# Optimization experiments

Measured on AMD Instinct MI355X. Metric: run time of the kernel, lower is better.

Reference implementation:

```python
import jax, jax.numpy as jnp
import numpy as np

B, N, S = 32, 4096, 11          # batch, n_inputs (64x64 feature map), n_slots
D_IN, D, MLP = 512, 512, 2048   # input feat dim, qkv_size, mlp hidden
ITERS = 3                       # num_iterations
EPS_ATTN = 1e-8                 # renormalize epsilon
EPS_LN = 1e-5                   # torch LayerNorm default eps


def layer_norm(x, g, b, eps=EPS_LN):
    mu = jnp.mean(x, axis=-1, keepdims=True)
    var = jnp.mean(jnp.square(x - mu), axis=-1, keepdims=True)
    return (x - mu) * jax.lax.rsqrt(var + eps) * g + b


def setup_inputs() -> dict:
    key = jax.random.key(0)
    ks = jax.random.split(key, 16)
    s = 0.02
    return {
        "slots": jax.random.normal(ks[0], (B, S, D), jnp.float32),
        "inputs": jax.random.normal(ks[1], (B, N, D_IN), jnp.float32),
        # input LayerNorm
        "ln_in_g": jnp.ones((D_IN,), jnp.float32),
        "ln_in_b": jnp.zeros((D_IN,), jnp.float32),
        # k / v projections (with bias, like nn.Linear)
        "Wk": jax.random.normal(ks[2], (D_IN, D), jnp.float32) * s,
        "bk": jnp.zeros((D,), jnp.float32),
        "Wv": jax.random.normal(ks[3], (D_IN, D), jnp.float32) * s,
        "bv": jnp.zeros((D,), jnp.float32),
        # query LayerNorm + bias-free q projection
        "ln_q_g": jnp.ones((D,), jnp.float32),
        "ln_q_b": jnp.zeros((D,), jnp.float32),
        "Wq": jax.random.normal(ks[4], (D, D), jnp.float32) * s,
        # GRUCell: gate order (r, z, n), torch layout [3D, D]
        "W_ih": jax.random.normal(ks[5], (3 * D, D), jnp.float32) * s,
        "b_ih": jnp.zeros((3 * D,), jnp.float32),
        "W_hh": jax.random.normal(ks[6], (3 * D, D), jnp.float32) * s,
        "b_hh": jnp.zeros((3 * D,), jnp.float32),
        # MLP: LN -> Linear -> ReLU -> Linear (no residual in source)
        "ln_m_g": jnp.ones((D,), jnp.float32),
        "ln_m_b": jnp.zeros((D,), jnp.float32),
        "W1": jax.random.normal(ks[7], (D, MLP), jnp.float32) * s,
        "b1": jnp.zeros((MLP,), jnp.float32),
        "W2": jax.random.normal(ks[8], (MLP, D), jnp.float32) * s,
        "b2": jnp.zeros((D,), jnp.float32),
    }


def reference(slots, inputs, ln_in_g, ln_in_b, Wk, bk, Wv, bv,
              ln_q_g, ln_q_b, Wq, W_ih, b_ih, W_hh, b_hh,
              ln_m_g, ln_m_b, W1, b1, W2, b2):
    # inputs LN + k/v projections (computed once, outside the loop)
    x = layer_norm(inputs, ln_in_g, ln_in_b)          # [B, N, D_IN]
    k = x @ Wk + bk                                   # [B, N, D]
    v = x @ Wv + bv                                   # [B, N, D]
    scale = 1.0 / jnp.sqrt(jnp.asarray(D, slots.dtype))

    for _ in range(ITERS):
        # q projection
        q = layer_norm(slots, ln_q_g, ln_q_b) @ Wq    # [B, S, D]
        # inverted attention: softmax over slot (query) axis
        logits = jnp.einsum('bsd,bnd->bsn', q * scale, k)  # [B, S, N]
        attn = jax.nn.softmax(logits, axis=-2)        # over S (inverted)
        # renormalize over keys (mean norm)
        attn = attn / (jnp.sum(attn, axis=-1, keepdims=True) + EPS_ATTN)
        updates = jnp.einsum('bsn,bnd->bsd', attn, v)  # [B, S, D]

        # GRUCell(updates, slots) -- torch semantics, gate order (r, z, n)
        gi = updates @ W_ih.T + b_ih                  # [B, S, 3D]
        gh = slots @ W_hh.T + b_hh                    # [B, S, 3D]
        ir, iz, in_ = jnp.split(gi, 3, axis=-1)
        hr, hz, hn = jnp.split(gh, 3, axis=-1)
        r = jax.nn.sigmoid(ir + hr)
        z = jax.nn.sigmoid(iz + hz)
        n = jnp.tanh(in_ + r * hn)
        slots = (1.0 - z) * n + z * slots

        # MLP (note: source assigns slots = mlp(slots), no residual)
        h = layer_norm(slots, ln_m_g, ln_m_b)
        slots = jax.nn.relu(h @ W1 + b1) @ W2 + b2
    return slots
```

## Files before the change

### kernel.cpp

```cpp
#include <hip/hip_runtime.h>
#include <cstdint>
#include <cstddef>

typedef short bf16x8 __attribute__((ext_vector_type(8)));
typedef float floatx4 __attribute__((ext_vector_type(4)));
typedef unsigned short ushort4v __attribute__((ext_vector_type(4)));

#define LN_EPS 1e-5f
#define ATTN_EPS 1e-8f
#define NCHUNK 16

__device__ __forceinline__ unsigned short f2bf(float f) {
    unsigned int u = __float_as_uint(f);
    u += 0x7fffu + ((u >> 16) & 1u);
    return (unsigned short)(u >> 16);
}

__device__ __forceinline__ void load_lds16(const void* gp, void* lp) {
    __builtin_amdgcn_global_load_lds(
        (__attribute__((address_space(1))) void*)gp,
        (__attribute__((address_space(3))) void*)lp,
        16, 0, 0);
}

template<bool OUT_BF16, bool QDOT>
__global__ __launch_bounds__(256) void ln512_kernel(
        const float* __restrict__ x, const float* __restrict__ g, const float* __restrict__ b,
        void* __restrict__ out, int total_rows, int data_rows, float outscale,
        const float* __restrict__ wqbk, float* __restrict__ cbuf) {
    int row = blockIdx.x * 4 + (threadIdx.x >> 6);
    int lane = threadIdx.x & 63;
    if (row >= total_rows) return;
    int rr = row < data_rows ? row : data_rows - 1;
    const float4* xr = (const float4*)(x + (size_t)rr * 512);
    float4 a0 = xr[lane];
    float4 a1 = xr[lane + 64];
    float s  = a0.x + a0.y + a0.z + a0.w + a1.x + a1.y + a1.z + a1.w;
    float ss = a0.x*a0.x + a0.y*a0.y + a0.z*a0.z + a0.w*a0.w
             + a1.x*a1.x + a1.y*a1.y + a1.z*a1.z + a1.w*a1.w;
    #pragma unroll
    for (int off = 32; off > 0; off >>= 1) {
        s  += __shfl_xor(s, off, 64);
        ss += __shfl_xor(ss, off, 64);
    }
    float mu = s * (1.0f / 512.0f);
    float var = ss * (1.0f / 512.0f) - mu * mu;
    float rstd = rsqrtf(var + LN_EPS);
    float4 g0 = ((const float4*)g)[lane];
    float4 g1 = ((const float4*)g)[lane + 64];
    float4 b0 = ((const float4*)b)[lane];
    float4 b1 = ((const float4*)b)[lane + 64];
    float y[8];
    y[0] = ((a0.x - mu) * rstd * g0.x + b0.x) * outscale;
    y[1] = ((a0.y - mu) * rstd * g0.y + b0.y) * outscale;
    y[2] = ((a0.z - mu) * rstd * g0.z + b0.z) * outscale;
    y[3] = ((a0.w - mu) * rstd * g0.w + b0.w) * outscale;
    y[4] = ((a1.x - mu) * rstd * g1.x + b1.x) * outscale;
    y[5] = ((a1.y - mu) * rstd * g1.y + b1.y) * outscale;
    y[6] = ((a1.z - mu) * rstd * g1.z + b1.z) * outscale;
    y[7] = ((a1.w - mu) * rstd * g1.w + b1.w) * outscale;
    if (QDOT) {
        float4 w0 = ((const float4*)wqbk)[lane];
        float4 w1 = ((const float4*)wqbk)[lane + 64];
        float cd = y[0]*w0.x + y[1]*w0.y + y[2]*w0.z + y[3]*w0.w
                 + y[4]*w1.x + y[5]*w1.y + y[6]*w1.z + y[7]*w1.w;
        #pragma unroll
        for (int off = 32; off > 0; off >>= 1) cd += __shfl_xor(cd, off, 64);
        if (lane == 0) cbuf[row] = cd;
    }
    if (OUT_BF16) {
        unsigned short* orow = (unsigned short*)out + (size_t)row * 512;
        ushort4v o0, o1;
        o0.x = f2bf(y[0]); o0.y = f2bf(y[1]); o0.z = f2bf(y[2]); o0.w = f2bf(y[3]);
        o1.x = f2bf(y[4]); o1.y = f2bf(y[5]); o1.z = f2bf(y[6]); o1.w = f2bf(y[7]);
        *(ushort4v*)(orow + lane * 4) = o0;
        *(ushort4v*)(orow + 256 + lane * 4) = o1;
    } else {
        float* orow = (float*)out + (size_t)row * 512;
        *(float4*)(orow + lane * 4) = make_float4(y[0], y[1], y[2], y[3]);
        *(float4*)(orow + 256 + lane * 4) = make_float4(y[4], y[5], y[6], y[7]);
    }
}

__device__ __forceinline__ void tr32(const float* __restrict__ in, unsigned short* __restrict__ out,
                                     int R, int C, int bx, int by, float (*tile)[33]) {
    int tx = threadIdx.x & 31, ty = threadIdx.x >> 5;
    #pragma unroll
    for (int i = 0; i < 32; i += 8)
        tile[ty + i][tx] = in[(size_t)(by + ty + i) * C + bx + tx];
    __syncthreads();
    #pragma unroll
    for (int i = 0; i < 32; i += 8)
        out[(size_t)(bx + ty + i) * R + by + tx] = f2bf(tile[tx][ty + i]);
}

__device__ __forceinline__ void rowdot512(const float* __restrict__ in, const float* __restrict__ vec,
                                          float* __restrict__ out, int row) {
    int lane = threadIdx.x & 63;
    const float4* r0 = (const float4*)(in + (size_t)row * 512);
    float4 a0 = r0[lane], a1 = r0[lane + 64];
    float4 v0 = ((const float4*)vec)[lane], v1 = ((const float4*)vec)[lane + 64];
    float d = a0.x*v0.x + a0.y*v0.y + a0.z*v0.z + a0.w*v0.w
            + a1.x*v1.x + a1.y*v1.y + a1.z*v1.z + a1.w*v1.w;
    #pragma unroll
    for (int off = 32; off > 0; off >>= 1) d += __shfl_xor(d, off, 64);
    if (lane == 0) out[row] = d;
}

__global__ __launch_bounds__(256) void prep_all(
        const float* __restrict__ Wk, const float* __restrict__ Wq,
        const float* __restrict__ Wv, const float* __restrict__ W_ih,
        const float* __restrict__ W_hh, const float* __restrict__ W1,
        const float* __restrict__ W2, const float* __restrict__ slots_in,
        const float* __restrict__ bk, const float* __restrict__ bv,
        unsigned short* __restrict__ Wk_b, unsigned short* __restrict__ Wq_b,
        unsigned short* __restrict__ Wv_b, unsigned short* __restrict__ Wih_b,
        unsigned short* __restrict__ Whh_b, unsigned short* __restrict__ W1T,
        unsigned short* __restrict__ W2T, unsigned short* __restrict__ slbf,
        float* __restrict__ wqbk, float* __restrict__ bvW, float* __restrict__ slots) {
    __shared__ float tile[32][33];
    const int b = blockIdx.x;
    const int t = threadIdx.x;
    if (b < 1024) {
        int idx = b * 256 + t; Wk_b[idx] = f2bf(Wk[idx]);
    } else if (b < 2048) {
        int idx = (b - 1024) * 256 + t; Wq_b[idx] = f2bf(Wq[idx]);
    } else if (b < 3072) {
        int idx = (b - 2048) * 256 + t; Wv_b[idx] = f2bf(Wv[idx]);
    } else if (b < 6144) {
        int idx = (b - 3072) * 256 + t; Wih_b[idx] = f2bf(W_ih[idx]);
    } else if (b < 9216) {
        int idx = (b - 6144) * 256 + t; Whh_b[idx] = f2bf(W_hh[idx]);
    } else if (b < 10240) {
        int i = b - 9216;
        tr32(W1, W1T, 512, 2048, (i & 63) * 32, (i >> 6) * 32, tile);
    } else if (b < 11264) {
        int i = b - 10240;
        tr32(W2, W2T, 2048, 512, (i & 15) * 32, (i >> 4) * 32, tile);
    } else if (b < 12032) {
        int idx = (b - 11264) * 256 + t;
        int row = idx >> 9, d = idx & 511;
        int rr = row < 352 ? row : 351;
        slbf[idx] = f2bf(slots_in[(size_t)rr * 512 + d]);
    } else if (b < 12160) {
        int row = (b - 12032) * 4 + (t >> 6);
        rowdot512(Wq, bk, wqbk, row);
    } else if (b < 12288) {
        int row = (b - 12160) * 4 + (t >> 6);
        rowdot512(W_ih, bv, bvW, row);
    } else {
        int idx = (b - 12288) * 256 + t;
        slots[idx] = slots_in[idx];
    }
}

template<int BMODE, bool RELU, int OUT_MODE>
__device__ __forceinline__ void hgemm_core(
        const unsigned short* __restrict__ A, const unsigned short* __restrict__ Bt,
        const float* __restrict__ bias, const float* __restrict__ bvW,
        const float* __restrict__ coef, float* __restrict__ Cf,
        unsigned short* __restrict__ Cb, int m0, int n0, int N, int K,
        unsigned short* As0, unsigned short* Bs0,
        unsigned short* As1, unsigned short* Bs1) {
    const int t = threadIdx.x;
    const int lane = t & 63;
    const int w = t >> 6;
    const int wm = w >> 1, wn = w & 1;
    const int quad = lane >> 4;
    const int l15 = lane & 15;
    floatx4 acc[2][2];
    #pragma unroll
    for (int i = 0; i < 2; ++i)
        #pragma unroll
        for (int j = 0; j < 2; ++j)
            #pragma unroll
            for (int r = 0; r < 4; ++r) acc[i][j][r] = 0.0f;

    auto stage = [&](unsigned short* Asd, unsigned short* Bsd, int k0) {
        #pragma unroll
        for (int p = 0; p < 2; ++p) {
            const int s = p * 256 + t;
            const int row = s >> 3;
            const int c = (s & 7) ^ (row & 7);
            const int ldsoff = (s - lane) * 16;
            load_lds16(A  + (size_t)(m0 + row) * K + k0 + c * 8, (char*)Asd + ldsoff);
            load_lds16(Bt + (size_t)(n0 + row) * K + k0 + c * 8, (char*)Bsd + ldsoff);
        }
    };
    auto compute = [&](const unsigned short* Asr, const unsigned short* Bsr) {
        #pragma unroll
        for (int h = 0; h < 2; ++h) {
            bf16x8 af[2], bfr[2];
            #pragma unroll
            for (int i = 0; i < 2; ++i) {
                const int row = wm * 32 + i * 16 + l15;
                const int cp = ((h << 2) | quad) ^ (l15 & 7);
                af[i] = *(const bf16x8*)(Asr + row * 64 + cp * 8);
            }
            #pragma unroll
            for (int j = 0; j < 2; ++j) {
                const int row = wn * 32 + j * 16 + l15;
                const int cp = ((h << 2) | quad) ^ (l15 & 7);
                bfr[j] = *(const bf16x8*)(Bsr + row * 64 + cp * 8);
            }
            #pragma unroll
            for (int i = 0; i < 2; ++i)
                #pragma unroll
                for (int j = 0; j < 2; ++j)
                    acc[i][j] = __builtin_amdgcn_mfma_f32_16x16x32_bf16(af[i], bfr[j], acc[i][j], 0, 0, 0);
        }
    };

    const int nk = K >> 6;
    stage(As0, Bs0, 0);
    for (int ki = 0; ki < nk; ++ki) {
        const bool odd = (ki & 1) != 0;
        unsigned short* Ac = odd ? As1 : As0;
        unsigned short* Bc = odd ? Bs1 : Bs0;
        if (ki + 1 < nk) {
            stage(odd ? As0 : As1, odd ? Bs0 : Bs1, (ki + 1) * 64);
            asm volatile("s_waitcnt vmcnt(4)" ::: "memory");
        } else {
            asm volatile("s_waitcnt vmcnt(0)" ::: "memory");
        }
        __builtin_amdgcn_s_barrier();
        __builtin_amdgcn_sched_barrier(0);
        compute(Ac, Bc);
        __builtin_amdgcn_sched_barrier(0);
        __builtin_amdgcn_s_barrier();
    }

    #pragma unroll
    for (int j = 0; j < 2; ++j) {
        const int n = n0 + wn * 32 + j * 16 + l15;
        const float bb = (BMODE >= 1) ? bias[n] : 0.0f;
        const float bw = (BMODE == 2) ? bvW[n] : 0.0f;
        #pragma unroll
        for (int i = 0; i < 2; ++i) {
            #pragma unroll
            for (int r = 0; r < 4; ++r) {
                const int m = m0 + wm * 32 + i * 16 + quad * 4 + r;
                float v = acc[i][j][r] + bb;
                if (BMODE == 2) v += coef[m] * bw;
                if (RELU) v = fmaxf(v, 0.0f);
                if (OUT_MODE == 0 || OUT_MODE == 2) Cf[(size_t)m * N + n] = v;
                if (OUT_MODE == 1 || OUT_MODE == 2) Cb[(size_t)m * N + n] = f2bf(v);
            }
        }
    }
}

template<int BMODE, bool RELU, int OUT_MODE>
__global__ __launch_bounds__(256) void hgemm(
        const unsigned short* __restrict__ A, const unsigned short* __restrict__ Bt,
        const float* __restrict__ bias, float* __restrict__ Cf,
        unsigned short* __restrict__ Cb, int N, int K) {
    __shared__ unsigned short As0[64 * 64];
    __shared__ unsigned short Bs0[64 * 64];
    __shared__ unsigned short As1[64 * 64];
    __shared__ unsigned short Bs1[64 * 64];
    hgemm_core<BMODE, RELU, OUT_MODE>(A, Bt, bias, nullptr, nullptr, Cf, Cb,
                                      blockIdx.y * 64, blockIdx.x * 64, N, K,
                                      As0, Bs0, As1, Bs1);
}

__global__ __launch_bounds__(256) void prep_gemms(
        const unsigned short* __restrict__ Wk_b, const unsigned short* __restrict__ Wq_b,
        const unsigned short* __restrict__ Wih_b, const unsigned short* __restrict__ Wv_b,
        unsigned short* __restrict__ WqkT, unsigned short* __restrict__ Wc) {
    __shared__ unsigned short As0[64 * 64];
    __shared__ unsigned short Bs0[64 * 64];
    __shared__ unsigned short As1[64 * 64];
    __shared__ unsigned short Bs1[64 * 64];
    if (blockIdx.z == 0) {
        if (blockIdx.y >= 8) return;
        hgemm_core<0, false, 1>(Wk_b, Wq_b, nullptr, nullptr, nullptr, nullptr, WqkT,
                                blockIdx.y * 64, blockIdx.x * 64, 512, 512,
                                As0, Bs0, As1, Bs1);
    } else {
        hgemm_core<0, false, 1>(Wih_b, Wv_b, nullptr, nullptr, nullptr, nullptr, Wc,
                                blockIdx.y * 64, blockIdx.x * 64, 512, 512,
                                As0, Bs0, As1, Bs1);
    }
}

__global__ __launch_bounds__(256) void gru_gemm(
        const unsigned short* __restrict__ Pn, const unsigned short* __restrict__ slbf,
        const unsigned short* __restrict__ Wc, const unsigned short* __restrict__ Whh,
        const float* __restrict__ bih, const float* __restrict__ bhh,
        const float* __restrict__ bvW, const float* __restrict__ coef,
        float* __restrict__ gi, float* __restrict__ gh) {
    __shared__ unsigned short As0[64 * 64];
    __shared__ unsigned short Bs0[64 * 64];
    __shared__ unsigned short As1[64 * 64];
    __shared__ unsigned short Bs1[64 * 64];
    if (blockIdx.z == 0)
        hgemm_core<2, false, 0>(Pn, Wc, bih, bvW, coef, gi, nullptr,
                                blockIdx.y * 64, blockIdx.x * 64, 1536, 512,
                                As0, Bs0, As1, Bs1);
    else
        hgemm_core<1, false, 0>(slbf, Whh, bhh, nullptr, nullptr, gh, nullptr,
                                blockIdx.y * 64, blockIdx.x * 64, 1536, 512,
                                As0, Bs0, As1, Bs1);
}

template<bool LN1>
__global__ __launch_bounds__(256, 3) void attn_kernel(
        const unsigned short* __restrict__ qp_b, unsigned short* xln,
        const float* __restrict__ cbuf,
        float* __restrict__ Up, float* __restrict__ rsp,
        const float* __restrict__ inputs,
        const float* __restrict__ ln_in_g, const float* __restrict__ ln_in_b) {
    const int b = blockIdx.y;
    const int chunk = blockIdx.x;
    const int w = threadIdx.x >> 6, lane = threadIdx.x & 63;
    const int l15 = lane & 15, quad = lane >> 4;
    const int NPC = 4096 / NCHUNK;

    __shared__ float P[64][20];
    __shared__ float rss[16];

    const size_t rowbase = (size_t)b * 4096 + (size_t)chunk * NPC;

    if (threadIdx.x < 16) rss[threadIdx.x] = 0.0f;

    if (LN1) {
        float4 g0 = ((const float4*)ln_in_g)[lane];
        float4 g1 = ((const float4*)ln_in_g)[lane + 64];
        float4 b0 = ((const float4*)ln_in_b)[lane];
        float4 b1 = ((const float4*)ln_in_b)[lane + 64];
        for (int r = w; r < NPC; r += 4) {
            const float4* xr = (const float4*)(inputs + (rowbase + r) * 512);
            float4 a0 = xr[lane];
            float4 a1 = xr[lane + 64];
            float s  = a0.x + a0.y + a0.z + a0.w + a1.x + a1.y + a1.z + a1.w;
            float ss = a0.x*a0.x + a0.y*a0.y + a0.z*a0.z + a0.w*a0.w
                     + a1.x*a1.x + a1.y*a1.y + a1.z*a1.z + a1.w*a1.w;
            #pragma unroll
            for (int off = 32; off > 0; off >>= 1) {
                s  += __shfl_xor(s, off, 64);
                ss += __shfl_xor(ss, off, 64);
            }
            float mu = s * (1.0f / 512.0f);
            float var = ss * (1.0f / 512.0f) - mu * mu;
            float rstd = rsqrtf(var + LN_EPS);
            unsigned short* orow = xln + (rowbase + r) * 512;
            ushort4v o0, o1;
            o0.x = f2bf((a0.x - mu) * rstd * g0.x + b0.x);
            o0.y = f2bf((a0.y - mu) * rstd * g0.y + b0.y);
            o0.z = f2bf((a0.z - mu) * rstd * g0.z + b0.z);
            o0.w = f2bf((a0.w - mu) * rstd * g0.w + b0.w);
            o1.x = f2bf((a1.x - mu) * rstd * g1.x + b1.x);
            o1.y = f2bf((a1.y - mu) * rstd * g1.y + b1.y);
            o1.z = f2bf((a1.z - mu) * rstd * g1.z + b1.z);
            o1.w = f2bf((a1.w - mu) * rstd * g1.w + b1.w);
            *(ushort4v*)(orow + lane * 4) = o0;
            *(ushort4v*)(orow + 256 + lane * 4) = o1;
        }
        __syncthreads();
    }

    const unsigned short* qrow = qp_b + (size_t)(b * 11 + (l15 < 11 ? l15 : 10)) * 512 + quad * 8;
    bf16x8 aq[16];
    #pragma unroll
    for (int ks = 0; ks < 16; ++ks) aq[ks] = *(const bf16x8*)(qrow + ks * 32);

    float cb[4];
    #pragma unroll
    for (int r = 0; r < 4; ++r) {
        int s = quad * 4 + r;
        cb[r] = (s < 11) ? cbuf[b * 11 + s] : 0.0f;
    }

    float U[11][2];
    #pragma unroll
    for (int s = 0; s < 11; ++s) { U[s][0] = 0.f; U[s][1] = 0.f; }
    float4 rsacc = make_float4(0.f, 0.f, 0.f, 0.f);

    const unsigned short* xbase = xln + rowbase * 512;
    const int d0 = w * 128 + lane * 2;

    for (int t = 0; t < NPC / 64; ++t) {
        const int n0 = t * 64 + w * 16;
        const unsigned short* krow = xbase + (size_t)(n0 + l15) * 512 + quad * 8;
        floatx4 ca, cb2;
        ca[0] = ca[1] = ca[2] = ca[3] = 0.0f;
        cb2[0] = cb2[1] = cb2[2] = cb2[3] = 0.0f;
        #pragma unroll
        for (int ks = 0; ks < 8; ++ks) {
            bf16x8 bf = *(const bf16x8*)(krow + ks * 32);
            ca = __builtin_amdgcn_mfma_f32_16x16x32_bf16(aq[ks], bf, ca, 0, 0, 0);
        }
        #pragma unroll
        for (int ks = 8; ks < 16; ++ks) {
            bf16x8 bf = *(const bf16x8*)(krow + ks * 32);
            cb2 = __builtin_amdgcn_mfma_f32_16x16x32_bf16(aq[ks], bf, cb2, 0, 0, 0);
        }
        float l0 = ca[0] + cb2[0] + cb[0], l1 = ca[1] + cb2[1] + cb[1];
        float l2 = ca[2] + cb2[2] + cb[2], l3 = ca[3] + cb2[3] + cb[3];
        if (quad == 2) l3 = -1e30f;
        if (quad == 3) { l0 = -1e30f; l1 = -1e30f; l2 = -1e30f; l3 = -1e30f; }
        float mx = fmaxf(fmaxf(l0, l1), fmaxf(l2, l3));
        mx = fmaxf(mx, __shfl_xor(mx, 16, 64));
        mx = fmaxf(mx, __shfl_xor(mx, 32, 64));
        float e0 = __expf(l0 - mx), e1 = __expf(l1 - mx),
              e2 = __expf(l2 - mx), e3 = __expf(l3 - mx);
        float se = e0 + e1 + e2 + e3;
        se += __shfl_xor(se, 16, 64);
        se += __shfl_xor(se, 32, 64);
        float inv = 1.0f / se;
        float4 av = make_float4(e0 * inv, e1 * inv, e2 * inv, e3 * inv);
        *(float4*)&P[w * 16 + l15][quad * 4] = av;
        float4 rv = av;
        #pragma unroll
        for (int off = 1; off < 16; off <<= 1) {
            rv.x += __shfl_xor(rv.x, off, 64);
            rv.y += __shfl_xor(rv.y, off, 64);
            rv.z += __shfl_xor(rv.z, off, 64);
            rv.w += __shfl_xor(rv.w, off, 64);
        }
        rsacc.x += rv.x; rsacc.y += rv.y; rsacc.z += rv.z; rsacc.w += rv.w;
        __syncthreads();

        const unsigned short* arow = xbase + (size_t)(t * 64) * 512 + d0;
        #pragma unroll 4
        for (int nl = 0; nl < 64; ++nl) {
            unsigned int kr = *(const unsigned int*)(arow + (size_t)nl * 512);
            float klo = __uint_as_float(kr << 16);
            float khi = __uint_as_float(kr & 0xffff0000u);
            const float* pr = &P[nl][0];
            float4 p0 = *(const float4*)(pr);
            float4 p1 = *(const float4*)(pr + 4);
            float4 p2 = *(const float4*)(pr + 8);
            float as[11] = {p0.x, p0.y, p0.z, p0.w, p1.x, p1.y, p1.z, p1.w,
                            p2.x, p2.y, p2.z};
            #pragma unroll
            for (int s = 0; s < 11; ++s) {
                U[s][0] = fmaf(as[s], klo, U[s][0]);
                U[s][1] = fmaf(as[s], khi, U[s][1]);
            }
        }
        __syncthreads();
    }

    float* up = Up + ((size_t)b * NCHUNK + chunk) * 11 * 512;
    #pragma unroll
    for (int s = 0; s < 11; ++s)
        *(float2*)(up + s * 512 + d0) = make_float2(U[s][0], U[s][1]);
    if (l15 == 0) {
        atomicAdd(&rss[quad * 4 + 0], rsacc.x);
        atomicAdd(&rss[quad * 4 + 1], rsacc.y);
        atomicAdd(&rss[quad * 4 + 2], rsacc.z);
        atomicAdd(&rss[quad * 4 + 3], rsacc.w);
    }
    __syncthreads();
    if (threadIdx.x < 11) rsp[((size_t)b * NCHUNK + chunk) * 11 + threadIdx.x] = rss[threadIdx.x];
}

__global__ __launch_bounds__(256) void attn_reduce(
        const float* __restrict__ Up, const float* __restrict__ rsp,
        unsigned short* __restrict__ Pn, float* __restrict__ coef) {
    const int bs = blockIdx.x;
    if (bs >= 352) {
        for (int d = threadIdx.x; d < 512; d += 256) Pn[(size_t)bs * 512 + d] = 0;
        if (threadIdx.x == 0) coef[bs] = 0.0f;
        return;
    }
    const int b = bs / 11, s = bs - b * 11;
    float rsum = 0.0f;
    #pragma unroll
    for (int c = 0; c < NCHUNK; ++c) rsum += rsp[((size_t)b * NCHUNK + c) * 11 + s];
    const float inv = 1.0f / (rsum + ATTN_EPS);
    if (threadIdx.x == 0) coef[bs] = rsum * inv;
    for (int d = threadIdx.x; d < 512; d += 256) {
        float acc = 0.f;
        #pragma unroll
        for (int c = 0; c < NCHUNK; ++c) acc += Up[(((size_t)b * NCHUNK + c) * 11 + s) * 512 + d];
        Pn[(size_t)bs * 512 + d] = f2bf(acc * inv);
    }
}

__global__ __launch_bounds__(256) void gru_ln(
        const float* __restrict__ gi, const float* __restrict__ gh,
        const float* __restrict__ slots, const float* __restrict__ g,
        const float* __restrict__ b, unsigned short* __restrict__ mln) {
    int row = blockIdx.x * 4 + (threadIdx.x >> 6);
    int lane = threadIdx.x & 63;
    unsigned short* orow = mln + (size_t)row * 512;
    if (row >= 352) {
        ushort4v z; z.x = z.y = z.z = z.w = 0;
        *(ushort4v*)(orow + lane * 4) = z;
        *(ushort4v*)(orow + 256 + lane * 4) = z;
        return;
    }
    const float4* gir = (const float4*)(gi + (size_t)row * 1536);
    const float4* ghr = (const float4*)(gh + (size_t)row * 1536);
    const float4* sr  = (const float4*)(slots + (size_t)row * 512);
    float v[8];
    #pragma unroll
    for (int half = 0; half < 2; ++half) {
        int o = half * 64 + lane;
        float4 ir = gir[o], iz = gir[128 + o], in_ = gir[256 + o];
        float4 hr = ghr[o], hz = ghr[128 + o], hn = ghr[256 + o];
        float4 sv = sr[o];
        float rr[4], zz[4], nn[4];
        rr[0] = 1.f / (1.f + __expf(-(ir.x + hr.x)));
        rr[1] = 1.f / (1.f + __expf(-(ir.y + hr.y)));
        rr[2] = 1.f / (1.f + __expf(-(ir.z + hr.z)));
        rr[3] = 1.f / (1.f + __expf(-(ir.w + hr.w)));
        zz[0] = 1.f / (1.f + __expf(-(iz.x + hz.x)));
        zz[1] = 1.f / (1.f + __expf(-(iz.y + hz.y)));
        zz[2] = 1.f / (1.f + __expf(-(iz.z + hz.z)));
        zz[3] = 1.f / (1.f + __expf(-(iz.w + hz.w)));
        nn[0] = tanhf(in_.x + rr[0] * hn.x);
        nn[1] = tanhf(in_.y + rr[1] * hn.y);
        nn[2] = tanhf(in_.z + rr[2] * hn.z);
        nn[3] = tanhf(in_.w + rr[3] * hn.w);
        v[half * 4 + 0] = (1.f - zz[0]) * nn[0] + zz[0] * sv.x;
        v[half * 4 + 1] = (1.f - zz[1]) * nn[1] + zz[1] * sv.y;
        v[half * 4 + 2] = (1.f - zz[2]) * nn[2] + zz[2] * sv.z;
        v[half * 4 + 3] = (1.f - zz[3]) * nn[3] + zz[3] * sv.w;
    }
    float s = 0.f, ss = 0.f;
    #pragma unroll
    for (int j = 0; j < 8; ++j) { s += v[j]; ss += v[j] * v[j]; }
    #pragma unroll
    for (int off = 32; off > 0; off >>= 1) {
        s  += __shfl_xor(s, off, 64);
        ss += __shfl_xor(ss, off, 64);
    }
    float mu = s * (1.0f / 512.0f);
    float var = ss * (1.0f / 512.0f) - mu * mu;
    float rstd = rsqrtf(var + LN_EPS);
    float4 g0 = ((const float4*)g)[lane], g1 = ((const float4*)g)[lane + 64];
    float4 b0 = ((const float4*)b)[lane], b1 = ((const float4*)b)[lane + 64];
    ushort4v o0, o1;
    o0.x = f2bf((v[0] - mu) * rstd * g0.x + b0.x);
    o0.y = f2bf((v[1] - mu) * rstd * g0.y + b0.y);
    o0.z = f2bf((v[2] - mu) * rstd * g0.z + b0.z);
    o0.w = f2bf((v[3] - mu) * rstd * g0.w + b0.w);
    o1.x = f2bf((v[4] - mu) * rstd * g1.x + b1.x);
    o1.y = f2bf((v[5] - mu) * rstd * g1.y + b1.y);
    o1.z = f2bf((v[6] - mu) * rstd * g1.z + b1.z);
    o1.w = f2bf((v[7] - mu) * rstd * g1.w + b1.w);
    *(ushort4v*)(orow + lane * 4) = o0;
    *(ushort4v*)(orow + 256 + lane * 4) = o1;
}

extern "C" void kernel_launch(void* const* d_in, const int* in_sizes, int n_in,
                              void* d_out, int out_size, void* d_ws, size_t ws_size,
                              hipStream_t stream) {
    const float* slots_in = (const float*)d_in[0];
    const float* inputs   = (const float*)d_in[1];
    const float* ln_in_g  = (const float*)d_in[2];
    const float* ln_in_b  = (const float*)d_in[3];
    const float* Wk  = (const float*)d_in[4];
    const float* bk  = (const float*)d_in[5];
    const float* Wv  = (const float*)d_in[6];
    const float* bv  = (const float*)d_in[7];
    const float* ln_q_g = (const float*)d_in[8];
    const float* ln_q_b = (const float*)d_in[9];
    const float* Wq  = (const float*)d_in[10];
    const float* W_ih = (const float*)d_in[11];
    const float* b_ih = (const float*)d_in[12];
    const float* W_hh = (const float*)d_in[13];
    const float* b_hh = (const float*)d_in[14];
    const float* ln_m_g = (const float*)d_in[15];
    const float* ln_m_b = (const float*)d_in[16];
    const float* W1 = (const float*)d_in[17];
    const float* b1 = (const float*)d_in[18];
    const float* W2 = (const float*)d_in[19];
    const float* b2 = (const float*)d_in[20];

    char* p = (char*)d_ws;
    auto alloc = [&](size_t bytes) { char* r = p; p += (bytes + 255) & ~(size_t)255; return r; };
    unsigned short* xln   = (unsigned short*)alloc(131072ull * 512 * 2);
    unsigned short* Wk_b  = (unsigned short*)alloc(512ull * 512 * 2);
    unsigned short* Wq_b  = (unsigned short*)alloc(512ull * 512 * 2);
    unsigned short* Wv_b  = (unsigned short*)alloc(512ull * 512 * 2);
    unsigned short* Wih_b = (unsigned short*)alloc(1536ull * 512 * 2);
    unsigned short* Whh_b = (unsigned short*)alloc(1536ull * 512 * 2);
    unsigned short* WqkT  = (unsigned short*)alloc(512ull * 512 * 2);
    unsigned short* Wc    = (unsigned short*)alloc(1536ull * 512 * 2);
    unsigned short* W1T   = (unsigned short*)alloc(2048ull * 512 * 2);
    unsigned short* W2T   = (unsigned short*)alloc(512ull * 2048 * 2);
    unsigned short* slq   = (unsigned short*)alloc(384ull * 512 * 2);
    unsigned short* mln   = (unsigned short*)alloc(384ull * 512 * 2);
    unsigned short* Pn    = (unsigned short*)alloc(384ull * 512 * 2);
    unsigned short* slbf  = (unsigned short*)alloc(384ull * 512 * 2);
    unsigned short* h1    = (unsigned short*)alloc(384ull * 2048 * 2);
    unsigned short* qp_b  = (unsigned short*)alloc(384ull * 512 * 2);
    float* slots = (float*)alloc(384ull * 512 * 4);
    float* gi    = (float*)alloc(384ull * 1536 * 4);
    float* gh    = (float*)alloc(384ull * 1536 * 4);
    float* Up    = (float*)alloc((size_t)32 * NCHUNK * 11 * 512 * 4);
    float* rsp   = (float*)alloc((size_t)32 * NCHUNK * 11 * 4);
    float* wqbk  = (float*)alloc(512 * 4);
    float* bvW   = (float*)alloc(1536 * 4);
    float* cbuf  = (float*)alloc(384 * 4);
    float* coef  = (float*)alloc(384 * 4);

    prep_all<<<dim3(12992), 256, 0, stream>>>(
        Wk, Wq, Wv, W_ih, W_hh, W1, W2, slots_in, bk, bv,
        Wk_b, Wq_b, Wv_b, Wih_b, Whh_b, W1T, W2T, slbf, wqbk, bvW, slots);
    prep_gemms<<<dim3(8, 24, 2), 256, 0, stream>>>(Wk_b, Wq_b, Wih_b, Wv_b, WqkT, Wc);

    const float qscale = 0.044194173824159216f;
    for (int it = 0; it < 3; ++it) {
        ln512_kernel<true, true><<<dim3(96), 256, 0, stream>>>(
            slots, ln_q_g, ln_q_b, slq, 384, 352, qscale, wqbk, cbuf);
        hgemm<0, false, 1><<<dim3(8, 6), 256, 0, stream>>>(slq, WqkT, nullptr, nullptr, qp_b, 512, 512);
        if (it == 0)
            attn_kernel<true><<<dim3(NCHUNK, 32), 256, 0, stream>>>(
                qp_b, xln, cbuf, Up, rsp, inputs, ln_in_g, ln_in_b);
        else
            attn_kernel<false><<<dim3(NCHUNK, 32), 256, 0, stream>>>(
                qp_b, xln, cbuf, Up, rsp, nullptr, nullptr, nullptr);
        attn_reduce<<<dim3(384), 256, 0, stream>>>(Up, rsp, Pn, coef);
        gru_gemm<<<dim3(24, 6, 2), 256, 0, stream>>>(Pn, slbf, Wc, Whh_b, b_ih, b_hh, bvW, coef, gi, gh);
        gru_ln<<<dim3(96), 256, 0, stream>>>(gi, gh, slots, ln_m_g, ln_m_b, mln);
        hgemm<1, true, 1><<<dim3(32, 6), 256, 0, stream>>>(mln, W1T, b1, nullptr, h1, 2048, 512);
        hgemm<1, false, 2><<<dim3(8, 6), 256, 0, stream>>>(h1, W2T, b2, slots, slbf, 512, 2048);
    }
    hipMemcpyAsync(d_out, slots, (size_t)out_size * 4, hipMemcpyDeviceToDevice, stream);
}
```

Measured before the change: 843.3 us.

## Split attention accumulation per wave, stage queries in LDS, double chunk count

The attention kernel now has each wave accumulate updates only over its own 16 rows across all 512 feature dims (8 per lane), using wave barriers instead of block-wide syncs. Each wave writes its own partial sums, and the reduce kernel sums over four times as many partials. Query vectors are staged in swizzled LDS rather than held in registers, NCHUNK doubles to 32, and the occupancy hint rises to 4 blocks. The aim is to remove block-level synchronisation and raise parallelism and occupancy. The cost is 8x larger partial buffers and more work in the reduce kernel.

```diff
diff --git a/kernel.cpp b/kernel.cpp
--- a/kernel.cpp
+++ b/kernel.cpp
@@ -8,7 +8,7 @@
 
 #define LN_EPS 1e-5f
 #define ATTN_EPS 1e-8f
-#define NCHUNK 16
+#define NCHUNK 32
 
 __device__ __forceinline__ unsigned short f2bf(float f) {
     unsigned int u = __float_as_uint(f);
@@ -305,7 +305,7 @@
 }
 
 template<bool LN1>
-__global__ __launch_bounds__(256, 3) void attn_kernel(
+__global__ __launch_bounds__(256, 4) void attn_kernel(
         const unsigned short* __restrict__ qp_b, unsigned short* xln,
         const float* __restrict__ cbuf,
         float* __restrict__ Up, float* __restrict__ rsp,
@@ -315,14 +315,19 @@
     const int chunk = blockIdx.x;
     const int w = threadIdx.x >> 6, lane = threadIdx.x & 63;
     const int l15 = lane & 15, quad = lane >> 4;
+    const int d0 = lane * 8;
     const int NPC = 4096 / NCHUNK;
 
-    __shared__ float P[64][20];
-    __shared__ float rss[16];
-
+    __shared__ unsigned short Qs[11 * 512];
+    __shared__ float attnlds[4 * 16 * 20];
     const size_t rowbase = (size_t)b * 4096 + (size_t)chunk * NPC;
 
-    if (threadIdx.x < 16) rss[threadIdx.x] = 0.0f;
+    for (int i = threadIdx.x; i < 11 * 64; i += 256) {
+        int row = i >> 6, g = i & 63;
+        int gs = g ^ (row & 7);
+        *(uint4*)(Qs + (row * 64 + gs) * 8) =
+            *(const uint4*)(qp_b + (size_t)(b * 11 + row) * 512 + g * 8);
+    }
 
     if (LN1) {
         float4 g0 = ((const float4*)ln_in_g)[lane];
@@ -357,13 +362,8 @@
             *(ushort4v*)(orow + lane * 4) = o0;
             *(ushort4v*)(orow + 256 + lane * 4) = o1;
         }
-        __syncthreads();
-    }
-
-    const unsigned short* qrow = qp_b + (size_t)(b * 11 + (l15 < 11 ? l15 : 10)) * 512 + quad * 8;
-    bf16x8 aq[16];
-    #pragma unroll
-    for (int ks = 0; ks < 16; ++ks) aq[ks] = *(const bf16x8*)(qrow + ks * 32);
+    }
+    __syncthreads();
 
     float cb[4];
     #pragma unroll
@@ -372,13 +372,17 @@
         cb[r] = (s < 11) ? cbuf[b * 11 + s] : 0.0f;
     }
 
-    float U[11][2];
-    #pragma unroll
-    for (int s = 0; s < 11; ++s) { U[s][0] = 0.f; U[s][1] = 0.f; }
+    float U[11][8];
+    #pragma unroll
+    for (int s = 0; s < 11; ++s)
+        #pragma unroll
+        for (int j = 0; j < 8; ++j) U[s][j] = 0.f;
     float4 rsacc = make_float4(0.f, 0.f, 0.f, 0.f);
 
     const unsigned short* xbase = xln + rowbase * 512;
-    const int d0 = w * 128 + lane * 2;
+    const int rowq = (l15 < 11 ? l15 : 10);
+    const unsigned short* qlds = Qs + rowq * 512;
+    const int rsw = rowq & 7;
 
     for (int t = 0; t < NPC / 64; ++t) {
         const int n0 = t * 64 + w * 16;
@@ -388,13 +392,15 @@
         cb2[0] = cb2[1] = cb2[2] = cb2[3] = 0.0f;
         #pragma unroll
         for (int ks = 0; ks < 8; ++ks) {
+            bf16x8 aq = *(const bf16x8*)(qlds + (((ks * 4 + quad) ^ rsw) * 8));
             bf16x8 bf = *(const bf16x8*)(krow + ks * 32);
-            ca = __builtin_amdgcn_mfma_f32_16x16x32_bf16(aq[ks], bf, ca, 0, 0, 0);
+            ca = __builtin_amdgcn_mfma_f32_16x16x32_bf16(aq, bf, ca, 0, 0, 0);
         }
         #pragma unroll
         for (int ks = 8; ks < 16; ++ks) {
+            bf16x8 aq = *(const bf16x8*)(qlds + (((ks * 4 + quad) ^ rsw) * 8));
             bf16x8 bf = *(const bf16x8*)(krow + ks * 32);
-            cb2 = __builtin_amdgcn_mfma_f32_16x16x32_bf16(aq[ks], bf, cb2, 0, 0, 0);
+            cb2 = __builtin_amdgcn_mfma_f32_16x16x32_bf16(aq, bf, cb2, 0, 0, 0);
         }
         float l0 = ca[0] + cb2[0] + cb[0], l1 = ca[1] + cb2[1] + cb[1];
         float l2 = ca[2] + cb2[2] + cb[2], l3 = ca[3] + cb2[3] + cb[3];
@@ -410,7 +416,7 @@
         se += __shfl_xor(se, 32, 64);
         float inv = 1.0f / se;
         float4 av = make_float4(e0 * inv, e1 * inv, e2 * inv, e3 * inv);
-        *(float4*)&P[w * 16 + l15][quad * 4] = av;
+        *(float4*)&attnlds[(w * 16 + l15) * 20 + quad * 4] = av;
         float4 rv = av;
         #pragma unroll
         for (int off = 1; off < 16; off <<= 1) {
@@ -420,47 +426,50 @@
             rv.w += __shfl_xor(rv.w, off, 64);
         }
         rsacc.x += rv.x; rsacc.y += rv.y; rsacc.z += rv.z; rsacc.w += rv.w;
-        __syncthreads();
-
-        const unsigned short* arow = xbase + (size_t)(t * 64) * 512 + d0;
-        #pragma unroll 4
-        for (int nl = 0; nl < 64; ++nl) {
-            unsigned int kr = *(const unsigned int*)(arow + (size_t)nl * 512);
-            float klo = __uint_as_float(kr << 16);
-            float khi = __uint_as_float(kr & 0xffff0000u);
-            const float* pr = &P[nl][0];
-            float4 p0 = *(const float4*)(pr);
-            float4 p1 = *(const float4*)(pr + 4);
-            float4 p2 = *(const float4*)(pr + 8);
+        __builtin_amdgcn_wave_barrier();
+        for (int nl = 0; nl < 16; ++nl) {
+            uint4 kr = *(const uint4*)(xbase + (size_t)(n0 + nl) * 512 + d0);
+            float kf[8];
+            kf[0] = __uint_as_float(kr.x << 16); kf[1] = __uint_as_float(kr.x & 0xffff0000u);
+            kf[2] = __uint_as_float(kr.y << 16); kf[3] = __uint_as_float(kr.y & 0xffff0000u);
+            kf[4] = __uint_as_float(kr.z << 16); kf[5] = __uint_as_float(kr.z & 0xffff0000u);
+            kf[6] = __uint_as_float(kr.w << 16); kf[7] = __uint_as_float(kr.w & 0xffff0000u);
+            const float* arow = &attnlds[(w * 16 + nl) * 20];
+            float4 p0 = *(const float4*)(arow);
+            float4 p1 = *(const float4*)(arow + 4);
+            float4 p2 = *(const float4*)(arow + 8);
             float as[11] = {p0.x, p0.y, p0.z, p0.w, p1.x, p1.y, p1.z, p1.w,
                             p2.x, p2.y, p2.z};
             #pragma unroll
             for (int s = 0; s < 11; ++s) {
-                U[s][0] = fmaf(as[s], klo, U[s][0]);
-                U[s][1] = fmaf(as[s], khi, U[s][1]);
+                #pragma unroll
+                for (int j = 0; j < 8; ++j) U[s][j] = fmaf(as[s], kf[j], U[s][j]);
             }
         }
-        __syncthreads();
-    }
-
-    float* up = Up + ((size_t)b * NCHUNK + chunk) * 11 * 512;
-    #pragma unroll
-    for (int s = 0; s < 11; ++s)
-        *(float2*)(up + s * 512 + d0) = make_float2(U[s][0], U[s][1]);
+        __builtin_amdgcn_wave_barrier();
+    }
+
+    float* up = Up + ((size_t)((b * NCHUNK + chunk) * 4) + w) * 11 * 512;
+    #pragma unroll
+    for (int s = 0; s < 11; ++s) {
+        *(float4*)(up + s * 512 + d0)     = make_float4(U[s][0], U[s][1], U[s][2], U[s][3]);
+        *(float4*)(up + s * 512 + d0 + 4) = make_float4(U[s][4], U[s][5], U[s][6], U[s][7]);
+    }
     if (l15 == 0) {
-        atomicAdd(&rss[quad * 4 + 0], rsacc.x);
-        atomicAdd(&rss[quad * 4 + 1], rsacc.y);
-        atomicAdd(&rss[quad * 4 + 2], rsacc.z);
-        atomicAdd(&rss[quad * 4 + 3], rsacc.w);
-    }
-    __syncthreads();
-    if (threadIdx.x < 11) rsp[((size_t)b * NCHUNK + chunk) * 11 + threadIdx.x] = rss[threadIdx.x];
+        float* rw = rsp + ((size_t)((b * NCHUNK + chunk) * 4) + w) * 11;
+        int sb = quad * 4;
+        if (sb + 0 < 11) rw[sb + 0] = rsacc.x;
+        if (sb + 1 < 11) rw[sb + 1] = rsacc.y;
+        if (sb + 2 < 11) rw[sb + 2] = rsacc.z;
+        if (sb + 3 < 11) rw[sb + 3] = rsacc.w;
+    }
 }
 
 __global__ __launch_bounds__(256) void attn_reduce(
         const float* __restrict__ Up, const float* __restrict__ rsp,
         unsigned short* __restrict__ Pn, float* __restrict__ coef) {
     const int bs = blockIdx.x;
+    const int NP = NCHUNK * 4;
     if (bs >= 352) {
         for (int d = threadIdx.x; d < 512; d += 256) Pn[(size_t)bs * 512 + d] = 0;
         if (threadIdx.x == 0) coef[bs] = 0.0f;
@@ -468,14 +477,14 @@
     }
     const int b = bs / 11, s = bs - b * 11;
     float rsum = 0.0f;
-    #pragma unroll
-    for (int c = 0; c < NCHUNK; ++c) rsum += rsp[((size_t)b * NCHUNK + c) * 11 + s];
+    #pragma unroll 8
+    for (int c = 0; c < NP; ++c) rsum += rsp[((size_t)b * NP + c) * 11 + s];
     const float inv = 1.0f / (rsum + ATTN_EPS);
     if (threadIdx.x == 0) coef[bs] = rsum * inv;
     for (int d = threadIdx.x; d < 512; d += 256) {
         float acc = 0.f;
-        #pragma unroll
-        for (int c = 0; c < NCHUNK; ++c) acc += Up[(((size_t)b * NCHUNK + c) * 11 + s) * 512 + d];
+        #pragma unroll 8
+        for (int c = 0; c < NP; ++c) acc += Up[(((size_t)b * NP + c) * 11 + s) * 512 + d];
         Pn[(size_t)bs * 512 + d] = f2bf(acc * inv);
     }
 }
@@ -593,8 +602,8 @@
     float* slots = (float*)alloc(384ull * 512 * 4);
     float* gi    = (float*)alloc(384ull * 1536 * 4);
     float* gh    = (float*)alloc(384ull * 1536 * 4);
-    float* Up    = (float*)alloc((size_t)32 * NCHUNK * 11 * 512 * 4);
-    float* rsp   = (float*)alloc((size_t)32 * NCHUNK * 11 * 4);
+    float* Up    = (float*)alloc((size_t)32 * NCHUNK * 4 * 11 * 512 * 4);
+    float* rsp   = (float*)alloc((size_t)32 * NCHUNK * 4 * 11 * 4);
     float* wqbk  = (float*)alloc(512 * 4);
     float* bvW   = (float*)alloc(1536 * 4);
     float* cbuf  = (float*)alloc(384 * 4);
```

After: 979.1 us. 1.16x slower.
